# Optimization experiments

Measured on AMD Instinct MI355X. Metric: run time of the kernel, lower is better.

## Reference

```python
import jax, jax.numpy as jnp
import numpy as np

D = 256
H = 4
L = 6
N = 32768
NH = N // H  # 8192 per-head width
VOCAB = 256
B, T = 1, 1024
ROPE_BASE = 10000.0


def ln(x):
    # LayerNorm over last dim, no affine (elementwise_affine=False)
    m = jnp.mean(x, axis=-1, keepdims=True)
    v = jnp.var(x, axis=-1, keepdims=True)
    return (x - m) * jax.lax.rsqrt(v + 1e-5)


def rope(x):
    # standard rotary position embedding over the last dim (split-half convention)
    Dh = x.shape[-1]
    t = x.shape[-2]
    half = Dh // 2
    inv_freq = 1.0 / (ROPE_BASE ** (jnp.arange(half, dtype=jnp.float32) / half))
    ang = jnp.arange(t, dtype=jnp.float32)[:, None] * inv_freq[None, :]  # [T, half]
    cos, sin = jnp.cos(ang), jnp.sin(ang)
    x1, x2 = x[..., :half], x[..., half:]
    return jnp.concatenate([x1 * cos - x2 * sin, x2 * cos + x1 * sin], axis=-1)


def setup_inputs() -> dict:
    key = jax.random.key(0)
    ks = jax.random.split(key, 6)
    std = 0.02
    return {
        "idx": jax.random.randint(ks[0], (B, T), 0, VOCAB, dtype=jnp.int32),
        "wte": std * jax.random.normal(ks[1], (VOCAB, D), dtype=jnp.float32),
        "encoder": std * jax.random.normal(ks[2], (N, D), dtype=jnp.float32),
        "decoder_x": std * jax.random.normal(ks[3], (H, D, NH), dtype=jnp.float32),
        "decoder_y": std * jax.random.normal(ks[4], (H, D, NH), dtype=jnp.float32),
        "readout": std * jax.random.normal(ks[5], (D, VOCAB), dtype=jnp.float32),
    }


def reference(idx, wte, encoder, decoder_x, decoder_y, readout):
    b, t = idx.shape
    v = ln(wte[idx])  # [B, T, D]
    # strict causal mask (tril with diagonal=-1): position i attends to j < i
    mask = jnp.tril(jnp.ones((t, t), dtype=bool), k=-1)
    for _ in range(L):
        # x: relu(v @ decoder_x) -> [B, H, T, NH]
        x = jax.nn.relu(jnp.einsum('btd,hdn->bhtn', v, decoder_x))
        xr = rope(x)  # Q = K = x
        # unnormalized causal linear attention, strict lower triangular
        scores = jnp.einsum('bhtn,bhsn->bhts', xr, xr)
        scores = jnp.where(mask, scores, 0.0)
        a = jnp.einsum('bhts,bsd->bhtd', scores, v)  # V = v (broadcast over heads)
        # gated wide projection
        y = jax.nn.relu(jnp.einsum('bhtd,hdn->bhtn', ln(a), decoder_y)) * x
        # [B,H,T,NH] -> [B,T,H*NH] = [B,T,N]  (matches transpose(1,2).reshape)
        y = jnp.transpose(y, (0, 2, 1, 3)).reshape(b, t, N)
        v = ln(v + ln(y @ encoder))  # dropout is identity in eval
    return v @ readout  # [B, T, VOCAB]
```

## Files before the change

### kernel.cpp

```cpp
#include <hip/hip_runtime.h>
#include <hip/hip_bf16.h>
#include <stdint.h>

typedef unsigned short u16;
typedef unsigned int u32;
typedef __attribute__((ext_vector_type(8))) short i16x8;
typedef __attribute__((ext_vector_type(4))) float f32x4;

#define DEV __device__ __forceinline__

constexpr int T = 1024, D = 256, H = 4, NH = 8192, NF = 32768, HALF = 4096;

constexpr size_t OFF_DXT  = 0;
constexpr size_t OFF_DYT  = OFF_DXT  + (size_t)H*NH*D*2;
constexpr size_t OFF_ENCT = OFF_DYT  + (size_t)H*NH*D*2;
constexpr size_t OFF_ROT  = OFF_ENCT + (size_t)D*NF*2;
constexpr size_t OFF_COS  = OFF_ROT  + (size_t)D*D*2;
constexpr size_t OFF_SIN  = OFF_COS  + (size_t)T*HALF*4;
constexpr size_t OFF_V    = OFF_SIN  + (size_t)T*HALF*4;
constexpr size_t OFF_VBF  = OFF_V    + (size_t)T*D*4;
constexpr size_t OFF_VT   = OFF_VBF  + (size_t)T*D*2;
constexpr size_t OFF_X    = OFF_VT   + (size_t)T*D*2;
constexpr size_t OFF_XR   = OFF_X    + (size_t)T*NF*2;
constexpr size_t OFF_SC   = OFF_XR   + (size_t)T*NF*2;
constexpr size_t OFF_LA   = OFF_SC   + (size_t)H*T*T*2;
constexpr size_t OFF_PART = OFF_LA   + (size_t)H*T*D*2;
constexpr size_t WS_NEED  = OFF_PART + (size_t)8*T*T*4;

DEV u16 f2bf(float f) {
  u32 u = __float_as_uint(f);
  u += 0x7FFFu + ((u >> 16) & 1u);
  return (u16)(u >> 16);
}
DEV float bf2f(u16 u) { return __uint_as_float(((u32)u) << 16); }

DEV float2 block_sum2(float a, float b, float* sb) {
  #pragma unroll
  for (int o = 32; o > 0; o >>= 1) {
    a += __shfl_down(a, o, 64);
    b += __shfl_down(b, o, 64);
  }
  const int w = threadIdx.x >> 6;
  __syncthreads();
  if ((threadIdx.x & 63) == 0) { sb[w*2] = a; sb[w*2+1] = b; }
  __syncthreads();
  return make_float2(sb[0]+sb[2]+sb[4]+sb[6], sb[1]+sb[3]+sb[5]+sb[7]);
}

DEV void stage128(const u16* __restrict__ g, int ld, char* lds, int wave, int lane) {
  #pragma unroll
  for (int i = 0; i < 4; ++i) {
    const int f = (wave*4 + i)*64 + lane;
    const int row = f >> 3, seg = f & 7;
    const int segl = seg ^ (row & 7);
    const u16* src = g + (size_t)row*ld + segl*8;
    __builtin_amdgcn_global_load_lds(
        (const __attribute__((address_space(1))) void*)src,
        (__attribute__((address_space(3))) void*)(lds + ((wave*4 + i) << 10)),
        16, 0, 0);
  }
}

DEV void gemm_bt_core(const u16* __restrict__ Ab, int lda,
                      const u16* __restrict__ Bb, int ldb,
                      int nkt, char* smem, f32x4 acc[4][4]) {
  const int tid = threadIdx.x, lane = tid & 63, wave = tid >> 6;
  const int wm = wave >> 1, wn = wave & 1;
  const int lr = lane & 15, lk = lane >> 4;
  char* As = smem;
  char* Bs = smem + 32768;
  #pragma unroll
  for (int m = 0; m < 4; ++m)
    #pragma unroll
    for (int n = 0; n < 4; ++n) acc[m][n] = f32x4{0.f, 0.f, 0.f, 0.f};
  stage128(Ab, lda, As, wave, lane);
  stage128(Bb, ldb, Bs, wave, lane);
  __syncthreads();
  for (int kt = 0; kt < nkt; ++kt) {
    const int cur = kt & 1;
    if (kt + 1 < nkt) {
      stage128(Ab + (size_t)(kt+1)*64, lda, As + ((cur^1) << 14), wave, lane);
      stage128(Bb + (size_t)(kt+1)*64, ldb, Bs + ((cur^1) << 14), wave, lane);
    }
    const char* Ac = As + (cur << 14);
    const char* Bc = Bs + (cur << 14);
    #pragma unroll
    for (int kk = 0; kk < 2; ++kk) {
      const int lcol = kk*64 + lk*16;
      i16x8 af[4], bfv[4];
      #pragma unroll
      for (int m = 0; m < 4; ++m) {
        const int row = wm*64 + m*16 + lr;
        af[m] = *(const i16x8*)(Ac + row*128 + (lcol ^ ((row & 7) << 4)));
      }
      #pragma unroll
      for (int n = 0; n < 4; ++n) {
        const int row = wn*64 + n*16 + lr;
        bfv[n] = *(const i16x8*)(Bc + row*128 + (lcol ^ ((row & 7) << 4)));
      }
      #pragma unroll
      for (int m = 0; m < 4; ++m)
        #pragma unroll
        for (int n = 0; n < 4; ++n)
          acc[m][n] = __builtin_amdgcn_mfma_f32_16x16x32_bf16(af[m], bfv[n], acc[m][n], 0, 0, 0);
    }
    __syncthreads();
  }
}

#define EPILOG_IDX() \
  const int lane = threadIdx.x & 63, wave = threadIdx.x >> 6; \
  const int wm = wave >> 1, wn = wave & 1, lr = lane & 15, lk = lane >> 4; \
  const int r0 = wm*64 + lk*4; \
  const int c0 = wn*64 + lr;

__global__ __launch_bounds__(256) void k_transpose_cvt(const float* __restrict__ in,
                                                       u16* __restrict__ out, int R, int C) {
  __shared__ float tile[32][33];
  const size_t zoff = (size_t)blockIdx.z * R * C;
  const float* inz = in + zoff;
  u16* outz = out + zoff;
  const int c0 = blockIdx.x << 5, rr0 = blockIdx.y << 5;
  const int tx = threadIdx.x & 31, ty = threadIdx.x >> 5;
  #pragma unroll
  for (int i = 0; i < 4; ++i)
    tile[ty + i*8][tx] = inz[(size_t)(rr0 + ty + i*8)*C + c0 + tx];
  __syncthreads();
  #pragma unroll
  for (int i = 0; i < 4; ++i) {
    const int rr = ty + i*8;
    outz[(size_t)(c0 + rr)*R + rr0 + tx] = f2bf(tile[tx][rr]);
  }
}

__global__ __launch_bounds__(256) void k_rope_table(float* __restrict__ cosT,
                                                    float* __restrict__ sinT) {
  const int i = blockIdx.x*256 + threadIdx.x;
  const int t = blockIdx.y;
  const float p = (float)i * (1.f/4096.f);
  const float ang = (float)t * expf(-9.210340371976184f * p);
  cosT[(size_t)t*HALF + i] = cosf(ang);
  sinT[(size_t)t*HALF + i] = sinf(ang);
}

__global__ __launch_bounds__(256) void k_embed(const int* __restrict__ idx,
                                               const float* __restrict__ wte,
                                               float* __restrict__ v,
                                               u16* __restrict__ vbf, u16* __restrict__ vT) {
  __shared__ float sb[8];
  const int t = blockIdx.x, d = threadIdx.x;
  const float val = wte[(size_t)idx[t]*D + d];
  float2 ss = block_sum2(val, val*val, sb);
  const float m = ss.x*(1.f/256.f), var = ss.y*(1.f/256.f) - m*m;
  const float vn = (val - m) * rsqrtf(var + 1e-5f);
  v[(size_t)t*D + d] = vn;
  const u16 b = f2bf(vn);
  vbf[(size_t)t*D + d] = b;
  vT[(size_t)d*T + t] = b;
}

__global__ __launch_bounds__(256) void k_gemm_x(const u16* __restrict__ vbf,
                                                const u16* __restrict__ dxT,
                                                u16* __restrict__ x) {
  __shared__ char smem[65536];
  const int nt = blockIdx.x, mt = blockIdx.y, h = blockIdx.z;
  f32x4 acc[4][4];
  gemm_bt_core(vbf + (size_t)mt*128*D, D,
               dxT + ((size_t)h*NH + (size_t)nt*128)*D, D, 4, smem, acc);
  EPILOG_IDX();
  const int tb = mt*128 + r0;
  const size_t cb = (size_t)h*NH + (size_t)nt*128 + c0;
  #pragma unroll
  for (int m = 0; m < 4; ++m)
    #pragma unroll
    for (int n = 0; n < 4; ++n)
      #pragma unroll
      for (int r = 0; r < 4; ++r)
        x[(size_t)(tb + m*16 + r)*NF + cb + n*16] = f2bf(fmaxf(acc[m][n][r], 0.f));
}

__global__ __launch_bounds__(256) void k_rope(const u16* __restrict__ x, u16* __restrict__ xr,
                                              const float* __restrict__ cosT,
                                              const float* __restrict__ sinT) {
  const size_t id = (size_t)blockIdx.x*256 + threadIdx.x;
  const int i4 = (int)(id & 1023), h = (int)((id >> 10) & 3), t = (int)(id >> 12);
  const size_t o1 = (size_t)t*NF + (size_t)h*NH + (size_t)i4*4;
  const ushort4 a = *(const ushort4*)(x + o1);
  const ushort4 b = *(const ushort4*)(x + o1 + HALF);
  const float4 c = *(const float4*)(cosT + (size_t)t*HALF + i4*4);
  const float4 s = *(const float4*)(sinT + (size_t)t*HALF + i4*4);
  ushort4 r1, r2;
  float x1, x2;
  x1 = bf2f(a.x); x2 = bf2f(b.x); r1.x = f2bf(x1*c.x - x2*s.x); r2.x = f2bf(x2*c.x + x1*s.x);
  x1 = bf2f(a.y); x2 = bf2f(b.y); r1.y = f2bf(x1*c.y - x2*s.y); r2.y = f2bf(x2*c.y + x1*s.y);
  x1 = bf2f(a.z); x2 = bf2f(b.z); r1.z = f2bf(x1*c.z - x2*s.z); r2.z = f2bf(x2*c.z + x1*s.z);
  x1 = bf2f(a.w); x2 = bf2f(b.w); r1.w = f2bf(x1*c.w - x2*s.w); r2.w = f2bf(x2*c.w + x1*s.w);
  *(ushort4*)(xr + o1) = r1;
  *(ushort4*)(xr + o1 + HALF) = r2;
}

__global__ __launch_bounds__(256) void k_gemm_sc(const u16* __restrict__ xr,
                                                 float* __restrict__ scpart) {
  __shared__ char smem[65536];
  const int z = blockIdx.x & 7;
  const int i = blockIdx.x >> 3;
  int tt = 0;
  while ((tt + 1)*(tt + 2)/2 <= i) ++tt;
  const int st = i - tt*(tt + 1)/2;
  const int h = z >> 1, kc = z & 1;
  const u16* base = xr + (size_t)h*NH + (size_t)kc*4096;
  f32x4 acc[4][4];
  gemm_bt_core(base + (size_t)tt*128*NF, NF, base + (size_t)st*128*NF, NF, 64, smem, acc);
  EPILOG_IDX();
  float* Cp = scpart + (size_t)z * T * T;
  const int tb = tt*128 + r0, sb_ = st*128 + c0;
  #pragma unroll
  for (int m = 0; m < 4; ++m)
    #pragma unroll
    for (int n = 0; n < 4; ++n)
      #pragma unroll
      for (int r = 0; r < 4; ++r)
        Cp[(size_t)(tb + m*16 + r)*T + sb_ + n*16] = acc[m][n][r];
}

__global__ __launch_bounds__(256) void k_sc_combine(const float* __restrict__ scpart,
                                                    u16* __restrict__ sc) {
  const int row = blockIdx.x;
  const int h = row >> 10, t = row & 1023;
  const float* p0 = scpart + ((size_t)(h*2 + 0)*T + t)*T;
  const float* p1 = scpart + ((size_t)(h*2 + 1)*T + t)*T;
  u16* o = sc + (size_t)row*T;
  const int s0 = threadIdx.x*4;
  ushort4 r;
  if (s0 >= t) {
    r.x = 0; r.y = 0; r.z = 0; r.w = 0;
  } else {
    const float4 a = *(const float4*)(p0 + s0);
    const float4 b = *(const float4*)(p1 + s0);
    r.x = f2bf((s0 + 0 < t) ? a.x + b.x : 0.f);
    r.y = f2bf((s0 + 1 < t) ? a.y + b.y : 0.f);
    r.z = f2bf((s0 + 2 < t) ? a.z + b.z : 0.f);
    r.w = f2bf((s0 + 3 < t) ? a.w + b.w : 0.f);
  }
  *(ushort4*)(o + s0) = r;
}

__global__ __launch_bounds__(256) void k_gemm_av(const u16* __restrict__ sc,
                                                 const u16* __restrict__ vT,
                                                 float* __restrict__ part) {
  __shared__ char smem[65536];
  const int slot = blockIdx.x & 7;
  const int h = slot >> 1, nt = slot & 1;
  int mt = 0, kc = 0, rem = blockIdx.x >> 3;
  #pragma unroll
  for (int m = 0; m < 8; ++m) {
    const int c = (m >> 1) + 1;
    if (rem < c) { mt = m; kc = rem; break; }
    rem -= c;
  }
  f32x4 acc[4][4];
  gemm_bt_core(sc + ((size_t)h*T + (size_t)mt*128)*T + (size_t)kc*256, T,
               vT + (size_t)nt*128*T + (size_t)kc*256, T, 4, smem, acc);
  EPILOG_IDX();
  float* Cp = part + (size_t)(h*4 + kc) * T * D;
  const int tb = mt*128 + r0, cb = nt*128 + c0;
  #pragma unroll
  for (int m = 0; m < 4; ++m)
    #pragma unroll
    for (int n = 0; n < 4; ++n)
      #pragma unroll
      for (int r = 0; r < 4; ++r)
        Cp[(size_t)(tb + m*16 + r)*D + cb + n*16] = acc[m][n][r];
}

__global__ __launch_bounds__(256) void k_ln_a(const float* __restrict__ part,
                                              u16* __restrict__ la) {
  __shared__ float sb[8];
  const int row = blockIdx.x;
  const int h = row >> 10, t = row & 1023;
  const int d = threadIdx.x;
  const int nkc = ((t >> 7) >> 1) + 1;
  float s = 0.f;
  for (int kc = 0; kc < nkc; ++kc)
    s += part[((size_t)(h*4 + kc)*T + t)*D + d];
  float2 ss = block_sum2(s, s*s, sb);
  const float m = ss.x*(1.f/256.f), var = ss.y*(1.f/256.f) - m*m;
  la[(size_t)row*D + d] = f2bf((s - m) * rsqrtf(var + 1e-5f));
}

__global__ __launch_bounds__(256) void k_gemm_y(const u16* __restrict__ la,
                                                const u16* __restrict__ dyT,
                                                const u16* __restrict__ x,
                                                u16* __restrict__ y) {
  __shared__ char smem[65536];
  const int nt = blockIdx.x, mt = blockIdx.y, h = blockIdx.z;
  f32x4 acc[4][4];
  gemm_bt_core(la + ((size_t)h*T + (size_t)mt*128)*D, D,
               dyT + ((size_t)h*NH + (size_t)nt*128)*D, D, 4, smem, acc);
  EPILOG_IDX();
  const int tb = mt*128 + r0;
  const size_t cb = (size_t)h*NH + (size_t)nt*128 + c0;
  #pragma unroll
  for (int m = 0; m < 4; ++m)
    #pragma unroll
    for (int n = 0; n < 4; ++n)
      #pragma unroll
      for (int r = 0; r < 4; ++r) {
        const size_t o = (size_t)(tb + m*16 + r)*NF + cb + n*16;
        const float xv = bf2f(x[o]);
        y[o] = f2bf(fmaxf(acc[m][n][r], 0.f) * xv);
      }
}

__global__ __launch_bounds__(256) void k_gemm_enc(const u16* __restrict__ y,
                                                  const u16* __restrict__ encT,
                                                  float* __restrict__ part) {
  __shared__ char smem[65536];
  const int slot = blockIdx.x & 7;
  const int seq  = blockIdx.x >> 3;
  const int kc = slot*2 + (seq >> 4);
  const int nt = seq & 1;
  const int mt = (seq >> 1) & 7;
  f32x4 acc[4][4];
  gemm_bt_core(y + (size_t)mt*128*NF + (size_t)kc*2048, NF,
               encT + (size_t)nt*128*NF + (size_t)kc*2048, NF, 32, smem, acc);
  EPILOG_IDX();
  float* Cp = part + (size_t)kc * T * D;
  const int tb = mt*128 + r0, cb = nt*128 + c0;
  #pragma unroll
  for (int m = 0; m < 4; ++m)
    #pragma unroll
    for (int n = 0; n < 4; ++n)
      #pragma unroll
      for (int r = 0; r < 4; ++r)
        Cp[(size_t)(tb + m*16 + r)*D + cb + n*16] = acc[m][n][r];
}

__global__ __launch_bounds__(256) void k_newv(const float* __restrict__ part,
                                              float* __restrict__ v,
                                              u16* __restrict__ vbf, u16* __restrict__ vT) {
  __shared__ float sb[8];
  const int t = blockIdx.x, d = threadIdx.x;
  float s = 0.f;
  #pragma unroll
  for (int kc = 0; kc < 16; ++kc)
    s += part[((size_t)kc*T + t)*D + d];
  float2 ss = block_sum2(s, s*s, sb);
  float m = ss.x*(1.f/256.f), var = ss.y*(1.f/256.f) - m*m;
  const float l1 = (s - m) * rsqrtf(var + 1e-5f);
  const float u = v[(size_t)t*D + d] + l1;
  float2 s2 = block_sum2(u, u*u, sb);
  m = s2.x*(1.f/256.f); var = s2.y*(1.f/256.f) - m*m;
  const float vn = (u - m) * rsqrtf(var + 1e-5f);
  v[(size_t)t*D + d] = vn;
  const u16 bb = f2bf(vn);
  vbf[(size_t)t*D + d] = bb;
  vT[(size_t)d*T + t] = bb;
}

__global__ __launch_bounds__(256) void k_gemm_out(const u16* __restrict__ vbf,
                                                  const u16* __restrict__ roT,
                                                  float* __restrict__ out) {
  __shared__ char smem[65536];
  const int nt = blockIdx.x, mt = blockIdx.y;
  f32x4 acc[4][4];
  gemm_bt_core(vbf + (size_t)mt*128*D, D, roT + (size_t)nt*128*D, D, 4, smem, acc);
  EPILOG_IDX();
  const int tb = mt*128 + r0, cb = nt*128 + c0;
  #pragma unroll
  for (int m = 0; m < 4; ++m)
    #pragma unroll
    for (int n = 0; n < 4; ++n)
      #pragma unroll
      for (int r = 0; r < 4; ++r)
        out[(size_t)(tb + m*16 + r)*D + cb + n*16] = acc[m][n][r];
}

extern "C" void kernel_launch(void* const* d_in, const int* in_sizes, int n_in,
                              void* d_out, int out_size, void* d_ws, size_t ws_size,
                              hipStream_t stream) {
  (void)in_sizes; (void)n_in; (void)out_size; (void)ws_size;
  const int*   idx = (const int*)d_in[0];
  const float* wte = (const float*)d_in[1];
  const float* enc = (const float*)d_in[2];
  const float* dx  = (const float*)d_in[3];
  const float* dy  = (const float*)d_in[4];
  const float* ro  = (const float*)d_in[5];
  float* out = (float*)d_out;
  char* ws = (char*)d_ws;

  u16* dxT  = (u16*)(ws + OFF_DXT);
  u16* dyT  = (u16*)(ws + OFF_DYT);
  u16* encT = (u16*)(ws + OFF_ENCT);
  u16* roT  = (u16*)(ws + OFF_ROT);
  float* cosT = (float*)(ws + OFF_COS);
  float* sinT = (float*)(ws + OFF_SIN);
  float* v    = (float*)(ws + OFF_V);
  u16* vbf  = (u16*)(ws + OFF_VBF);
  u16* vT   = (u16*)(ws + OFF_VT);
  u16* x    = (u16*)(ws + OFF_X);
  u16* xr   = (u16*)(ws + OFF_XR);
  u16* sc   = (u16*)(ws + OFF_SC);
  u16* la   = (u16*)(ws + OFF_LA);
  float* scpart = (float*)(ws + OFF_PART);
  float* part   = (float*)(ws + OFF_PART);

  k_transpose_cvt<<<dim3(NH/32, D/32, H), 256, 0, stream>>>(dx, dxT, D, NH);
  k_transpose_cvt<<<dim3(NH/32, D/32, H), 256, 0, stream>>>(dy, dyT, D, NH);
  k_transpose_cvt<<<dim3(D/32, NF/32, 1), 256, 0, stream>>>(enc, encT, NF, D);
  k_transpose_cvt<<<dim3(D/32, D/32, 1), 256, 0, stream>>>(ro, roT, D, D);
  k_rope_table<<<dim3(HALF/256, T), 256, 0, stream>>>(cosT, sinT);
  k_embed<<<T, 256, 0, stream>>>(idx, wte, v, vbf, vT);

  for (int l = 0; l < 6; ++l) {
    k_gemm_x  <<<dim3(64, 8, H),   256, 0, stream>>>(vbf, dxT, x);
    k_rope    <<<16384,            256, 0, stream>>>(x, xr, cosT, sinT);
    k_gemm_sc <<<288,              256, 0, stream>>>(xr, scpart);
    k_sc_combine<<<H*T,            256, 0, stream>>>(scpart, sc);
    k_gemm_av <<<160,              256, 0, stream>>>(sc, vT, part);
    k_ln_a    <<<H*T,              256, 0, stream>>>(part, la);
    k_gemm_y  <<<dim3(64, 8, H),   256, 0, stream>>>(la, dyT, x, xr );
    k_gemm_enc<<<256,              256, 0, stream>>>(xr , encT, part);
    k_newv    <<<T,                256, 0, stream>>>(part, v, vbf, vT);
  }
  k_gemm_out<<<dim3(2, 8), 256, 0, stream>>>(vbf, roT, out);
}
```

Baseline: 1.320 ms.

## Fuse RoPE into x-projection GEMM epilogue and deepen encoder split-K

The x-projection GEMM now computes both rotary halves in one block, with two accumulator sets, and applies RoPE in the epilogue. This writes both x and xr directly and removes the standalone rope kernel's full reread of x. The cos/sin tables are transposed so each thread loads a float4 along the time axis. Separately, the encoder GEMM split-K goes from 16 to 32 chunks with twice as many blocks, and the combine step sums 32 partials. The costs are higher register pressure from two accumulator sets, scattered 2-byte stores, and more partial-sum traffic.

```diff
diff --git a/kernel.cpp b/kernel.cpp
--- a/kernel.cpp
+++ b/kernel.cpp
@@ -135,12 +135,12 @@
 
 __global__ __launch_bounds__(256) void k_rope_table(float* __restrict__ cosT,
                                                     float* __restrict__ sinT) {
-  const int i = blockIdx.x*256 + threadIdx.x;
-  const int t = blockIdx.y;
+  const int t = blockIdx.x*256 + threadIdx.x;
+  const int i = blockIdx.y;
   const float p = (float)i * (1.f/4096.f);
   const float ang = (float)t * expf(-9.210340371976184f * p);
-  cosT[(size_t)t*HALF + i] = cosf(ang);
-  sinT[(size_t)t*HALF + i] = sinf(ang);
+  cosT[(size_t)i*T + t] = cosf(ang);
+  sinT[(size_t)i*T + t] = sinf(ang);
 }
 
 __global__ __launch_bounds__(256) void k_embed(const int* __restrict__ idx,
@@ -159,44 +159,44 @@
   vT[(size_t)d*T + t] = b;
 }
 
-__global__ __launch_bounds__(256) void k_gemm_x(const u16* __restrict__ vbf,
-                                                const u16* __restrict__ dxT,
-                                                u16* __restrict__ x) {
+__global__ __launch_bounds__(256) void k_gemm_x_rope(const u16* __restrict__ vbf,
+                                                     const u16* __restrict__ dxT,
+                                                     u16* __restrict__ x,
+                                                     u16* __restrict__ xr,
+                                                     const float* __restrict__ cosT,
+                                                     const float* __restrict__ sinT) {
   __shared__ char smem[65536];
   const int nt = blockIdx.x, mt = blockIdx.y, h = blockIdx.z;
-  f32x4 acc[4][4];
+  f32x4 acc1[4][4], acc2[4][4];
   gemm_bt_core(vbf + (size_t)mt*128*D, D,
-               dxT + ((size_t)h*NH + (size_t)nt*128)*D, D, 4, smem, acc);
+               dxT + ((size_t)h*NH + (size_t)nt*128)*D, D, 4, smem, acc1);
+  gemm_bt_core(vbf + (size_t)mt*128*D, D,
+               dxT + ((size_t)h*NH + HALF + (size_t)nt*128)*D, D, 4, smem, acc2);
   EPILOG_IDX();
   const int tb = mt*128 + r0;
-  const size_t cb = (size_t)h*NH + (size_t)nt*128 + c0;
-  #pragma unroll
-  for (int m = 0; m < 4; ++m)
-    #pragma unroll
-    for (int n = 0; n < 4; ++n)
-      #pragma unroll
-      for (int r = 0; r < 4; ++r)
-        x[(size_t)(tb + m*16 + r)*NF + cb + n*16] = f2bf(fmaxf(acc[m][n][r], 0.f));
-}
-
-__global__ __launch_bounds__(256) void k_rope(const u16* __restrict__ x, u16* __restrict__ xr,
-                                              const float* __restrict__ cosT,
-                                              const float* __restrict__ sinT) {
-  const size_t id = (size_t)blockIdx.x*256 + threadIdx.x;
-  const int i4 = (int)(id & 1023), h = (int)((id >> 10) & 3), t = (int)(id >> 12);
-  const size_t o1 = (size_t)t*NF + (size_t)h*NH + (size_t)i4*4;
-  const ushort4 a = *(const ushort4*)(x + o1);
-  const ushort4 b = *(const ushort4*)(x + o1 + HALF);
-  const float4 c = *(const float4*)(cosT + (size_t)t*HALF + i4*4);
-  const float4 s = *(const float4*)(sinT + (size_t)t*HALF + i4*4);
-  ushort4 r1, r2;
-  float x1, x2;
-  x1 = bf2f(a.x); x2 = bf2f(b.x); r1.x = f2bf(x1*c.x - x2*s.x); r2.x = f2bf(x2*c.x + x1*s.x);
-  x1 = bf2f(a.y); x2 = bf2f(b.y); r1.y = f2bf(x1*c.y - x2*s.y); r2.y = f2bf(x2*c.y + x1*s.y);
-  x1 = bf2f(a.z); x2 = bf2f(b.z); r1.z = f2bf(x1*c.z - x2*s.z); r2.z = f2bf(x2*c.z + x1*s.z);
-  x1 = bf2f(a.w); x2 = bf2f(b.w); r1.w = f2bf(x1*c.w - x2*s.w); r2.w = f2bf(x2*c.w + x1*s.w);
-  *(ushort4*)(xr + o1) = r1;
-  *(ushort4*)(xr + o1 + HALF) = r2;
+  #pragma unroll
+  for (int m = 0; m < 4; ++m) {
+    #pragma unroll
+    for (int n = 0; n < 4; ++n) {
+      const int i = nt*128 + c0 + n*16;
+      const float4 cv = *(const float4*)(cosT + (size_t)i*T + tb + m*16);
+      const float4 sv = *(const float4*)(sinT + (size_t)i*T + tb + m*16);
+      #pragma unroll
+      for (int r = 0; r < 4; ++r) {
+        const int t = tb + m*16 + r;
+        const float c = (r == 0) ? cv.x : (r == 1) ? cv.y : (r == 2) ? cv.z : cv.w;
+        const float s = (r == 0) ? sv.x : (r == 1) ? sv.y : (r == 2) ? sv.z : sv.w;
+        const u16 x1u = f2bf(fmaxf(acc1[m][n][r], 0.f));
+        const u16 x2u = f2bf(fmaxf(acc2[m][n][r], 0.f));
+        const float x1 = bf2f(x1u), x2 = bf2f(x2u);
+        const size_t o = (size_t)t*NF + (size_t)h*NH + i;
+        x[o]         = x1u;
+        x[o + HALF]  = x2u;
+        xr[o]        = f2bf(x1*c - x2*s);
+        xr[o + HALF] = f2bf(x2*c + x1*s);
+      }
+    }
+  }
 }
 
 __global__ __launch_bounds__(256) void k_gemm_sc(const u16* __restrict__ xr,
@@ -318,14 +318,14 @@
   __shared__ char smem[65536];
   const int slot = blockIdx.x & 7;
   const int seq  = blockIdx.x >> 3;
-  const int kc = slot*2 + (seq >> 4);
+  const int kcc = slot*4 + (seq >> 4);
   const int nt = seq & 1;
   const int mt = (seq >> 1) & 7;
   f32x4 acc[4][4];
-  gemm_bt_core(y + (size_t)mt*128*NF + (size_t)kc*2048, NF,
-               encT + (size_t)nt*128*NF + (size_t)kc*2048, NF, 32, smem, acc);
-  EPILOG_IDX();
-  float* Cp = part + (size_t)kc * T * D;
+  gemm_bt_core(y + (size_t)mt*128*NF + (size_t)kcc*1024, NF,
+               encT + (size_t)nt*128*NF + (size_t)kcc*1024, NF, 16, smem, acc);
+  EPILOG_IDX();
+  float* Cp = part + (size_t)kcc * T * D;
   const int tb = mt*128 + r0, cb = nt*128 + c0;
   #pragma unroll
   for (int m = 0; m < 4; ++m)
@@ -343,7 +343,7 @@
   const int t = blockIdx.x, d = threadIdx.x;
   float s = 0.f;
   #pragma unroll
-  for (int kc = 0; kc < 16; ++kc)
+  for (int kc = 0; kc < 32; ++kc)
     s += part[((size_t)kc*T + t)*D + d];
   float2 ss = block_sum2(s, s*s, sb);
   float m = ss.x*(1.f/256.f), var = ss.y*(1.f/256.f) - m*m;
@@ -409,18 +409,17 @@
   k_transpose_cvt<<<dim3(NH/32, D/32, H), 256, 0, stream>>>(dy, dyT, D, NH);
   k_transpose_cvt<<<dim3(D/32, NF/32, 1), 256, 0, stream>>>(enc, encT, NF, D);
   k_transpose_cvt<<<dim3(D/32, D/32, 1), 256, 0, stream>>>(ro, roT, D, D);
-  k_rope_table<<<dim3(HALF/256, T), 256, 0, stream>>>(cosT, sinT);
+  k_rope_table<<<dim3(T/256, HALF), 256, 0, stream>>>(cosT, sinT);
   k_embed<<<T, 256, 0, stream>>>(idx, wte, v, vbf, vT);
 
   for (int l = 0; l < 6; ++l) {
-    k_gemm_x  <<<dim3(64, 8, H),   256, 0, stream>>>(vbf, dxT, x);
-    k_rope    <<<16384,            256, 0, stream>>>(x, xr, cosT, sinT);
+    k_gemm_x_rope<<<dim3(32, 8, H), 256, 0, stream>>>(vbf, dxT, x, xr, cosT, sinT);
     k_gemm_sc <<<288,              256, 0, stream>>>(xr, scpart);
     k_sc_combine<<<H*T,            256, 0, stream>>>(scpart, sc);
     k_gemm_av <<<160,              256, 0, stream>>>(sc, vT, part);
     k_ln_a    <<<H*T,              256, 0, stream>>>(part, la);
     k_gemm_y  <<<dim3(64, 8, H),   256, 0, stream>>>(la, dyT, x, xr );
-    k_gemm_enc<<<256,              256, 0, stream>>>(xr , encT, part);
+    k_gemm_enc<<<512,              256, 0, stream>>>(xr , encT, part);
     k_newv    <<<T,                256, 0, stream>>>(part, v, vbf, vT);
   }
   k_gemm_out<<<dim3(2, 8), 256, 0, stream>>>(vbf, roT, out);
```

After: 1.447 ms. 9.6% more time.

## Stage GEMM epilogues through LDS for coalesced stores and deepen split-K

Applied to the files above, without the earlier changes.

Adds a shared-memory staged epilogue that writes bf16 tiles with 16-byte coalesced stores, replacing scattered 2-byte stores in the x, y and score GEMMs. The y epilogue now loads the gating x vectorised. Split-K is doubled for the score GEMM (4 chunks, partials stored as bf16) and for the encoder GEMM (32 chunks), raising the grid size to fill more CUs. The cost is extra partial-buffer traffic and reduction work, plus bf16 rounding of the score partials before they are summed.

```diff
diff --git a/kernel.cpp b/kernel.cpp
--- a/kernel.cpp
+++ b/kernel.cpp
@@ -114,6 +114,39 @@
   const int r0 = wm*64 + lk*4; \
   const int c0 = wn*64 + lr;
 
+constexpr int TS = 136;
+template<int MODE>
+DEV void store_tile(const f32x4 acc[4][4], u16* __restrict__ dst, int ld,
+                    const u16* __restrict__ xg, char* smem) {
+  u16* tb = (u16*)smem;
+  EPILOG_IDX();
+  #pragma unroll
+  for (int m = 0; m < 4; ++m)
+    #pragma unroll
+    for (int n = 0; n < 4; ++n)
+      #pragma unroll
+      for (int r = 0; r < 4; ++r) {
+        float v = acc[m][n][r];
+        if (MODE >= 1) v = fmaxf(v, 0.f);
+        tb[(size_t)(r0 + m*16 + r)*TS + c0 + n*16] = f2bf(v);
+      }
+  __syncthreads();
+  const int rr = threadIdx.x >> 4;
+  const int cc = (threadIdx.x & 15)*8;
+  #pragma unroll
+  for (int it = 0; it < 8; ++it) {
+    const int row = it*16 + rr;
+    i16x8 w = *(const i16x8*)(tb + (size_t)row*TS + cc);
+    if (MODE == 2) {
+      const i16x8 xv = *(const i16x8*)(xg + (size_t)row*ld + cc);
+      #pragma unroll
+      for (int j = 0; j < 8; ++j)
+        w[j] = (short)f2bf(bf2f((u16)w[j]) * bf2f((u16)xv[j]));
+    }
+    *(i16x8*)(dst + (size_t)row*ld + cc) = w;
+  }
+}
+
 __global__ __launch_bounds__(256) void k_transpose_cvt(const float* __restrict__ in,
                                                        u16* __restrict__ out, int R, int C) {
   __shared__ float tile[32][33];
@@ -167,16 +200,8 @@
   f32x4 acc[4][4];
   gemm_bt_core(vbf + (size_t)mt*128*D, D,
                dxT + ((size_t)h*NH + (size_t)nt*128)*D, D, 4, smem, acc);
-  EPILOG_IDX();
-  const int tb = mt*128 + r0;
-  const size_t cb = (size_t)h*NH + (size_t)nt*128 + c0;
-  #pragma unroll
-  for (int m = 0; m < 4; ++m)
-    #pragma unroll
-    for (int n = 0; n < 4; ++n)
-      #pragma unroll
-      for (int r = 0; r < 4; ++r)
-        x[(size_t)(tb + m*16 + r)*NF + cb + n*16] = f2bf(fmaxf(acc[m][n][r], 0.f));
+  store_tile<1>(acc, x + (size_t)mt*128*NF + (size_t)h*NH + (size_t)nt*128, NF,
+                nullptr, smem);
 }
 
 __global__ __launch_bounds__(256) void k_rope(const u16* __restrict__ x, u16* __restrict__ xr,
@@ -200,47 +225,44 @@
 }
 
 __global__ __launch_bounds__(256) void k_gemm_sc(const u16* __restrict__ xr,
-                                                 float* __restrict__ scpart) {
-  __shared__ char smem[65536];
-  const int z = blockIdx.x & 7;
-  const int i = blockIdx.x >> 3;
+                                                 u16* __restrict__ scb) {
+  __shared__ char smem[65536];
+  const int z = blockIdx.x & 15;
+  const int i = blockIdx.x >> 4;
   int tt = 0;
   while ((tt + 1)*(tt + 2)/2 <= i) ++tt;
   const int st = i - tt*(tt + 1)/2;
-  const int h = z >> 1, kc = z & 1;
-  const u16* base = xr + (size_t)h*NH + (size_t)kc*4096;
-  f32x4 acc[4][4];
-  gemm_bt_core(base + (size_t)tt*128*NF, NF, base + (size_t)st*128*NF, NF, 64, smem, acc);
-  EPILOG_IDX();
-  float* Cp = scpart + (size_t)z * T * T;
-  const int tb = tt*128 + r0, sb_ = st*128 + c0;
-  #pragma unroll
-  for (int m = 0; m < 4; ++m)
-    #pragma unroll
-    for (int n = 0; n < 4; ++n)
-      #pragma unroll
-      for (int r = 0; r < 4; ++r)
-        Cp[(size_t)(tb + m*16 + r)*T + sb_ + n*16] = acc[m][n][r];
-}
-
-__global__ __launch_bounds__(256) void k_sc_combine(const float* __restrict__ scpart,
+  const int h = z >> 2, kc = z & 3;
+  const u16* base = xr + (size_t)h*NH + (size_t)kc*2048;
+  f32x4 acc[4][4];
+  gemm_bt_core(base + (size_t)tt*128*NF, NF, base + (size_t)st*128*NF, NF, 32, smem, acc);
+  store_tile<0>(acc, scb + (size_t)z*T*T + (size_t)tt*128*T + (size_t)st*128, T,
+                nullptr, smem);
+}
+
+__global__ __launch_bounds__(256) void k_sc_combine(const u16* __restrict__ scb,
                                                     u16* __restrict__ sc) {
   const int row = blockIdx.x;
   const int h = row >> 10, t = row & 1023;
-  const float* p0 = scpart + ((size_t)(h*2 + 0)*T + t)*T;
-  const float* p1 = scpart + ((size_t)(h*2 + 1)*T + t)*T;
+  const u16* p0 = scb + ((size_t)(h*4 + 0)*T + t)*T;
   u16* o = sc + (size_t)row*T;
   const int s0 = threadIdx.x*4;
   ushort4 r;
   if (s0 >= t) {
     r.x = 0; r.y = 0; r.z = 0; r.w = 0;
   } else {
-    const float4 a = *(const float4*)(p0 + s0);
-    const float4 b = *(const float4*)(p1 + s0);
-    r.x = f2bf((s0 + 0 < t) ? a.x + b.x : 0.f);
-    r.y = f2bf((s0 + 1 < t) ? a.y + b.y : 0.f);
-    r.z = f2bf((s0 + 2 < t) ? a.z + b.z : 0.f);
-    r.w = f2bf((s0 + 3 < t) ? a.w + b.w : 0.f);
+    const ushort4 a0 = *(const ushort4*)(p0 + s0);
+    const ushort4 a1 = *(const ushort4*)(p0 + T*T + s0);
+    const ushort4 a2 = *(const ushort4*)(p0 + 2*(size_t)T*T + s0);
+    const ushort4 a3 = *(const ushort4*)(p0 + 3*(size_t)T*T + s0);
+    const float vx = bf2f(a0.x) + bf2f(a1.x) + bf2f(a2.x) + bf2f(a3.x);
+    const float vy = bf2f(a0.y) + bf2f(a1.y) + bf2f(a2.y) + bf2f(a3.y);
+    const float vz = bf2f(a0.z) + bf2f(a1.z) + bf2f(a2.z) + bf2f(a3.z);
+    const float vw = bf2f(a0.w) + bf2f(a1.w) + bf2f(a2.w) + bf2f(a3.w);
+    r.x = f2bf((s0 + 0 < t) ? vx : 0.f);
+    r.y = f2bf((s0 + 1 < t) ? vy : 0.f);
+    r.z = f2bf((s0 + 2 < t) ? vz : 0.f);
+    r.w = f2bf((s0 + 3 < t) ? vw : 0.f);
   }
   *(ushort4*)(o + s0) = r;
 }
@@ -297,19 +319,8 @@
   f32x4 acc[4][4];
   gemm_bt_core(la + ((size_t)h*T + (size_t)mt*128)*D, D,
                dyT + ((size_t)h*NH + (size_t)nt*128)*D, D, 4, smem, acc);
-  EPILOG_IDX();
-  const int tb = mt*128 + r0;
-  const size_t cb = (size_t)h*NH + (size_t)nt*128 + c0;
-  #pragma unroll
-  for (int m = 0; m < 4; ++m)
-    #pragma unroll
-    for (int n = 0; n < 4; ++n)
-      #pragma unroll
-      for (int r = 0; r < 4; ++r) {
-        const size_t o = (size_t)(tb + m*16 + r)*NF + cb + n*16;
-        const float xv = bf2f(x[o]);
-        y[o] = f2bf(fmaxf(acc[m][n][r], 0.f) * xv);
-      }
+  const size_t off = (size_t)mt*128*NF + (size_t)h*NH + (size_t)nt*128;
+  store_tile<2>(acc, y + off, NF, x + off, smem);
 }
 
 __global__ __launch_bounds__(256) void k_gemm_enc(const u16* __restrict__ y,
@@ -318,14 +329,14 @@
   __shared__ char smem[65536];
   const int slot = blockIdx.x & 7;
   const int seq  = blockIdx.x >> 3;
-  const int kc = slot*2 + (seq >> 4);
+  const int kcc = slot*4 + (seq >> 4);
   const int nt = seq & 1;
   const int mt = (seq >> 1) & 7;
   f32x4 acc[4][4];
-  gemm_bt_core(y + (size_t)mt*128*NF + (size_t)kc*2048, NF,
-               encT + (size_t)nt*128*NF + (size_t)kc*2048, NF, 32, smem, acc);
+  gemm_bt_core(y + (size_t)mt*128*NF + (size_t)kcc*1024, NF,
+               encT + (size_t)nt*128*NF + (size_t)kcc*1024, NF, 16, smem, acc);
   EPILOG_IDX();
-  float* Cp = part + (size_t)kc * T * D;
+  float* Cp = part + (size_t)kcc * T * D;
   const int tb = mt*128 + r0, cb = nt*128 + c0;
   #pragma unroll
   for (int m = 0; m < 4; ++m)
@@ -343,7 +354,7 @@
   const int t = blockIdx.x, d = threadIdx.x;
   float s = 0.f;
   #pragma unroll
-  for (int kc = 0; kc < 16; ++kc)
+  for (int kc = 0; kc < 32; ++kc)
     s += part[((size_t)kc*T + t)*D + d];
   float2 ss = block_sum2(s, s*s, sb);
   float m = ss.x*(1.f/256.f), var = ss.y*(1.f/256.f) - m*m;
@@ -402,8 +413,8 @@
   u16* xr   = (u16*)(ws + OFF_XR);
   u16* sc   = (u16*)(ws + OFF_SC);
   u16* la   = (u16*)(ws + OFF_LA);
-  float* scpart = (float*)(ws + OFF_PART);
-  float* part   = (float*)(ws + OFF_PART);
+  u16* scb  = (u16*)(ws + OFF_PART);
+  float* part = (float*)(ws + OFF_PART);
 
   k_transpose_cvt<<<dim3(NH/32, D/32, H), 256, 0, stream>>>(dx, dxT, D, NH);
   k_transpose_cvt<<<dim3(NH/32, D/32, H), 256, 0, stream>>>(dy, dyT, D, NH);
@@ -415,12 +426,12 @@
   for (int l = 0; l < 6; ++l) {
     k_gemm_x  <<<dim3(64, 8, H),   256, 0, stream>>>(vbf, dxT, x);
     k_rope    <<<16384,            256, 0, stream>>>(x, xr, cosT, sinT);
-    k_gemm_sc <<<288,              256, 0, stream>>>(xr, scpart);
-    k_sc_combine<<<H*T,            256, 0, stream>>>(scpart, sc);
+    k_gemm_sc <<<576,              256, 0, stream>>>(xr, scb);
+    k_sc_combine<<<H*T,            256, 0, stream>>>(scb, sc);
     k_gemm_av <<<160,              256, 0, stream>>>(sc, vT, part);
     k_ln_a    <<<H*T,              256, 0, stream>>>(part, la);
     k_gemm_y  <<<dim3(64, 8, H),   256, 0, stream>>>(la, dyT, x, xr );
-    k_gemm_enc<<<256,              256, 0, stream>>>(xr , encT, part);
+    k_gemm_enc<<<512,              256, 0, stream>>>(xr , encT, part);
     k_newv    <<<T,                256, 0, stream>>>(part, v, vbf, vT);
   }
   k_gemm_out<<<dim3(2, 8), 256, 0, stream>>>(vbf, roT, out);
```

After: 1.302 ms. Within noise of the previous version (-1.4%).
